# Optimization experiments

Measured on AMD Instinct MI355X. Metric: run time of the kernel, lower is better.

Reference implementation:

```python
import jax, jax.numpy as jnp
import numpy as np

N = 50000       # nodes
E = 1600000     # edges (before self loops)
IN = 128        # in_dim
H = 4           # heads
C = 64          # hidden_channels per head
F = H * C       # 256 concat width
OUT = 10
BN_EPS = 1e-5
NEG_SLOPE = 0.2  # PyG GATConv default


def _gat_conv(x, eidx, W, a_src, a_dst, b):
    # x: [N, F_in]; eidx: [2, E2] with self loops (row0=src, row1=dst)
    xw = (x @ W).reshape(N, H, C)                      # [N, H, C]
    s = jnp.einsum('nhc,hc->nh', xw, a_src)            # [N, H]
    d = jnp.einsum('nhc,hc->nh', xw, a_dst)            # [N, H]
    src, dst = eidx[0], eidx[1]
    alpha = jax.nn.leaky_relu(s[src] + d[dst], NEG_SLOPE)   # [E2, H]
    # scatter-softmax over incoming edges of each dst node (numerically stable)
    m = jax.ops.segment_max(alpha, dst, num_segments=N)
    m = jax.lax.stop_gradient(jnp.where(jnp.isfinite(m), m, 0.0))
    ex = jnp.exp(alpha - m[dst])                       # [E2, H]
    denom = jax.ops.segment_sum(ex, dst, num_segments=N)
    w = ex / (denom[dst] + 1e-16)                      # [E2, H]
    # weighted scatter-add aggregation
    out = jax.ops.segment_sum(w[:, :, None] * xw[src], dst, num_segments=N)  # [N,H,C]
    return out.reshape(N, F) + b


def _batchnorm(h, gamma, beta):
    # training-mode batch stats over the node axis
    mu = jnp.mean(h, axis=0)
    var = jnp.var(h, axis=0)
    return (h - mu) * jax.lax.rsqrt(var + BN_EPS) * gamma + beta


def setup_inputs() -> dict:
    key = jax.random.key(0)
    ks = jax.random.split(key, 12)
    sc = 0.05
    x = jax.random.normal(ks[0], (N, IN), jnp.float32)
    edge_index = jax.random.randint(ks[1], (2, E), 0, N, jnp.int64)
    return {
        'x': x,
        'edge_index': edge_index,
        'W1': jax.random.normal(ks[2], (IN, F), jnp.float32) * sc,
        'a_src1': jax.random.normal(ks[3], (H, C), jnp.float32) * sc,
        'a_dst1': jax.random.normal(ks[4], (H, C), jnp.float32) * sc,
        'b1': jnp.zeros((F,), jnp.float32),
        'W2': jax.random.normal(ks[5], (F, F), jnp.float32) * sc,
        'a_src2': jax.random.normal(ks[6], (H, C), jnp.float32) * sc,
        'a_dst2': jax.random.normal(ks[7], (H, C), jnp.float32) * sc,
        'b2': jnp.zeros((F,), jnp.float32),
        'g1': jnp.ones((F,), jnp.float32),
        'be1': jnp.zeros((F,), jnp.float32),
        'g2': jnp.ones((F,), jnp.float32),
        'be2': jnp.zeros((F,), jnp.float32),
        'Wc': jax.random.normal(ks[8], (F, OUT), jnp.float32) * sc,
        'bc': jnp.zeros((OUT,), jnp.float32),
    }


def reference(x, edge_index, W1, a_src1, a_dst1, b1, W2, a_src2, a_dst2, b2,
              g1, be1, g2, be2, Wc, bc):
    # add self loops (PyG GATConv default add_self_loops=True)
    loops = jnp.arange(N, dtype=edge_index.dtype)
    eidx = jnp.concatenate([edge_index, jnp.stack([loops, loops])], axis=1)
    h = jax.nn.relu(_gat_conv(x, eidx, W1, a_src1, a_dst1, b1))
    h = _batchnorm(h, g1, be1)          # dropout(0.2) treated as identity (eval)
    h = jax.nn.relu(_gat_conv(h, eidx, W2, a_src2, a_dst2, b2))
    h = _batchnorm(h, g2, be2)
    out = h @ Wc + bc                   # [N, OUT]
    return out[None]                    # [1, N, OUT]; squeeze(-1) is a no-op for OUT>1
```

## Files before the change

### kernel.cpp

```cpp
#include <hip/hip_runtime.h>

#define N_NODES 50000
#define E_EDGES 1600000
#define E2 (E_EDGES + N_NODES)
#define HEADS 4
#define F 256
#define OUTC 10
#define BN_EPS 1e-5f
#define NEG_SLOPE 0.2f
#define SB 1024
#define NB ((N_NODES + SB - 1) / SB)
#define NSLICE 64

static_assert(N_NODES % 4 == 0, "grid_nw exact");

typedef __attribute__((ext_vector_type(8))) short short8;
typedef __attribute__((ext_vector_type(4))) float f32x4;

__device__ __forceinline__ unsigned short f2bf(float f) {
    unsigned int u = __float_as_uint(f);
    unsigned int r = (u + 0x7fffu + ((u >> 16) & 1u)) >> 16;
    return (unsigned short)r;
}
__device__ __forceinline__ float bf2f(unsigned short b) {
    return __uint_as_float(((unsigned int)b) << 16);
}

__global__ __launch_bounds__(256) void convert_x(
    const float* __restrict__ X, unsigned short* __restrict__ Xb)
{
    int i = blockIdx.x * blockDim.x + threadIdx.x;
    const int total = N_NODES * 128 / 4;
    if (i >= total) return;
    float4 v = reinterpret_cast<const float4*>(X)[i];
    ushort4 o = { f2bf(v.x), f2bf(v.y), f2bf(v.z), f2bf(v.w) };
    reinterpret_cast<ushort4*>(Xb)[i] = o;
}

__global__ __launch_bounds__(256) void convert_w1T(
    const float* __restrict__ W1, unsigned short* __restrict__ WT)
{
    const int k = blockIdx.x;
    const int n = threadIdx.x;
    WT[n * 128 + k] = f2bf(W1[k * 256 + n]);
}

__global__ __launch_bounds__(256) void count_deg(
    const int* __restrict__ eidx, int* __restrict__ deg)
{
    int e = blockIdx.x * blockDim.x + threadIdx.x;
    if (e >= E2) return;
    int dst = (e < E_EDGES) ? eidx[E_EDGES + e] : e - E_EDGES;
    atomicAdd(&deg[dst], 1);
}

__global__ __launch_bounds__(SB) void scan_blocks(
    const int* __restrict__ deg, int* __restrict__ rowptr, int* __restrict__ bsum)
{
    __shared__ int sm[SB];
    const int t = threadIdx.x;
    const int idx = blockIdx.x * SB + t;
    int v = (idx < N_NODES) ? deg[idx] : 0;
    sm[t] = v;
    __syncthreads();
    for (int off = 1; off < SB; off <<= 1) {
        int u = (t >= off) ? sm[t - off] : 0;
        __syncthreads();
        sm[t] += u;
        __syncthreads();
    }
    if (idx < N_NODES) rowptr[idx] = sm[t] - v;
    if (t == SB - 1) bsum[blockIdx.x] = sm[t];
}

__global__ __launch_bounds__(64) void scan_bsums(
    const int* __restrict__ bsum, int* __restrict__ boff, int* __restrict__ rowptr)
{
    if (threadIdx.x == 0) {
        int run = 0;
        for (int b = 0; b < NB; b++) { boff[b] = run; run += bsum[b]; }
        rowptr[N_NODES] = run;
    }
}

__global__ __launch_bounds__(SB) void scan_add(
    int* __restrict__ rowptr, const int* __restrict__ boff)
{
    const int idx = blockIdx.x * SB + threadIdx.x;
    if (idx < N_NODES) rowptr[idx] += boff[blockIdx.x];
}

__global__ __launch_bounds__(256) void scatter_edges(
    const int* __restrict__ eidx, const int* __restrict__ rowptr,
    int* __restrict__ cursor, int* __restrict__ esrc)
{
    int e = blockIdx.x * blockDim.x + threadIdx.x;
    if (e >= E2) return;
    int src, dst;
    if (e < E_EDGES) { src = eidx[e]; dst = eidx[E_EDGES + e]; }
    else             { src = dst = e - E_EDGES; }
    int pos = atomicAdd(&cursor[dst], 1);
    esrc[rowptr[dst] + pos] = src;
}

template<int K, bool BROW>
__global__ __launch_bounds__(256) void gemm_sd(
    const unsigned short* __restrict__ A, const unsigned short* __restrict__ BT,
    const float* __restrict__ brow, const float* __restrict__ a_src,
    const float* __restrict__ a_dst, unsigned short* __restrict__ C,
    float* __restrict__ S, float* __restrict__ D)
{
    const int t = threadIdx.x;
    const int wave = t >> 6, lane = t & 63;
    const int lo = lane & 15, hi = lane >> 4;
    const int row0 = blockIdx.x * 64;
    const int nbase = wave * 64;

    int arow[4];
#pragma unroll
    for (int m = 0; m < 4; m++)
        arow[m] = min(row0 + m * 16 + lo, N_NODES - 1);

    f32x4 acc[4][4];
#pragma unroll
    for (int m = 0; m < 4; m++)
#pragma unroll
        for (int n = 0; n < 4; n++)
            acc[m][n] = (f32x4){0.f, 0.f, 0.f, 0.f};

    for (int k0 = 0; k0 < K; k0 += 32) {
        const int kk = k0 + hi * 8;
        short8 af[4], bfr[4];
#pragma unroll
        for (int m = 0; m < 4; m++)
            af[m] = *reinterpret_cast<const short8*>(A + (size_t)arow[m] * K + kk);
#pragma unroll
        for (int n = 0; n < 4; n++)
            bfr[n] = *reinterpret_cast<const short8*>(BT + (size_t)(nbase + n * 16 + lo) * K + kk);
#pragma unroll
        for (int m = 0; m < 4; m++)
#pragma unroll
            for (int n = 0; n < 4; n++)
                acc[m][n] = __builtin_amdgcn_mfma_f32_16x16x32_bf16(
                    af[m], bfr[n], acc[m][n], 0, 0, 0);
    }

    float bb[4], asv[4], adv[4];
#pragma unroll
    for (int n = 0; n < 4; n++) {
        int col = nbase + n * 16 + lo;
        bb[n]  = BROW ? brow[col] : 0.f;
        asv[n] = a_src[col];
        adv[n] = a_dst[col];
    }

#pragma unroll
    for (int m = 0; m < 4; m++) {
#pragma unroll
        for (int i = 0; i < 4; i++) {
            const int row = row0 + m * 16 + hi * 4 + i;
            const bool ok = row < N_NODES;
            float ps = 0.f, pd = 0.f;
#pragma unroll
            for (int n = 0; n < 4; n++) {
                float v = acc[m][n][i] + bb[n];
                ps += v * asv[n];
                pd += v * adv[n];
                if (ok) C[(size_t)row * F + nbase + n * 16 + lo] = f2bf(v);
            }
#pragma unroll
            for (int off = 1; off < 16; off <<= 1) {
                ps += __shfl_xor(ps, off, 64);
                pd += __shfl_xor(pd, off, 64);
            }
            if (lo == 0 && ok) {
                S[row * HEADS + wave] = ps;
                D[row * HEADS + wave] = pd;
            }
        }
    }
}

__global__ __launch_bounds__(256) void gat_aggregate(
    const int* __restrict__ rowptr, const int* __restrict__ esrc,
    const float* __restrict__ S, const float* __restrict__ D,
    const unsigned short* __restrict__ XWb, const float* __restrict__ bias,
    unsigned short* __restrict__ Hb, float* __restrict__ stp)
{
    __shared__ int   sbuf[4][64];
    __shared__ float wbuf[4][64][4];
    __shared__ float red_s[4][F];
    __shared__ float red_q[4][F];
    const int wv   = threadIdx.x >> 6;
    const int lane = threadIdx.x & 63;
    const int dst  = blockIdx.x * 4 + wv;
    const int beg = rowptr[dst], end = rowptr[dst + 1];
    const int h = lane >> 4;
    const float4 d4 = *reinterpret_cast<const float4*>(D + dst * HEADS);

    float ax = 0.f, ay = 0.f, az = 0.f, aw = 0.f, den = 0.f;

    for (int i = beg; i < end; i += 64) {
        const int nb = min(64, end - i);
        const bool valid = (i + lane < end);
        const int mysrc = valid ? esrc[i + lane] : 0;
        float4 w4 = {0.f, 0.f, 0.f, 0.f};
        if (valid) {
            const float4 s4 = *reinterpret_cast<const float4*>(S + mysrc * HEADS);
            float z;
            z = s4.x + d4.x; w4.x = __expf(z > 0.f ? z : NEG_SLOPE * z);
            z = s4.y + d4.y; w4.y = __expf(z > 0.f ? z : NEG_SLOPE * z);
            z = s4.z + d4.z; w4.z = __expf(z > 0.f ? z : NEG_SLOPE * z);
            z = s4.w + d4.w; w4.w = __expf(z > 0.f ? z : NEG_SLOPE * z);
        }
        sbuf[wv][lane] = mysrc;
        *reinterpret_cast<float4*>(&wbuf[wv][lane][0]) = w4;

        int j = 0;
        for (; j + 7 < nb; j += 8) {
            int s0 = sbuf[wv][j + 0], s1 = sbuf[wv][j + 1];
            int s2 = sbuf[wv][j + 2], s3 = sbuf[wv][j + 3];
            int s4i = sbuf[wv][j + 4], s5 = sbuf[wv][j + 5];
            int s6 = sbuf[wv][j + 6], s7 = sbuf[wv][j + 7];
            float w0 = wbuf[wv][j + 0][h], w1 = wbuf[wv][j + 1][h];
            float w2 = wbuf[wv][j + 2][h], w3 = wbuf[wv][j + 3][h];
            float w4f = wbuf[wv][j + 4][h], w5 = wbuf[wv][j + 5][h];
            float w6 = wbuf[wv][j + 6][h], w7 = wbuf[wv][j + 7][h];
            ushort4 x0 = *reinterpret_cast<const ushort4*>(XWb + (size_t)s0 * F + lane * 4);
            ushort4 x1 = *reinterpret_cast<const ushort4*>(XWb + (size_t)s1 * F + lane * 4);
            ushort4 x2 = *reinterpret_cast<const ushort4*>(XWb + (size_t)s2 * F + lane * 4);
            ushort4 x3 = *reinterpret_cast<const ushort4*>(XWb + (size_t)s3 * F + lane * 4);
            ushort4 x4 = *reinterpret_cast<const ushort4*>(XWb + (size_t)s4i * F + lane * 4);
            ushort4 x5 = *reinterpret_cast<const ushort4*>(XWb + (size_t)s5 * F + lane * 4);
            ushort4 x6 = *reinterpret_cast<const ushort4*>(XWb + (size_t)s6 * F + lane * 4);
            ushort4 x7 = *reinterpret_cast<const ushort4*>(XWb + (size_t)s7 * F + lane * 4);
            ax += w0 * bf2f(x0.x) + w1 * bf2f(x1.x) + w2 * bf2f(x2.x) + w3 * bf2f(x3.x)
                + w4f * bf2f(x4.x) + w5 * bf2f(x5.x) + w6 * bf2f(x6.x) + w7 * bf2f(x7.x);
            ay += w0 * bf2f(x0.y) + w1 * bf2f(x1.y) + w2 * bf2f(x2.y) + w3 * bf2f(x3.y)
                + w4f * bf2f(x4.y) + w5 * bf2f(x5.y) + w6 * bf2f(x6.y) + w7 * bf2f(x7.y);
            az += w0 * bf2f(x0.z) + w1 * bf2f(x1.z) + w2 * bf2f(x2.z) + w3 * bf2f(x3.z)
                + w4f * bf2f(x4.z) + w5 * bf2f(x5.z) + w6 * bf2f(x6.z) + w7 * bf2f(x7.z);
            aw += w0 * bf2f(x0.w) + w1 * bf2f(x1.w) + w2 * bf2f(x2.w) + w3 * bf2f(x3.w)
                + w4f * bf2f(x4.w) + w5 * bf2f(x5.w) + w6 * bf2f(x6.w) + w7 * bf2f(x7.w);
            den += ((w0 + w1) + (w2 + w3)) + ((w4f + w5) + (w6 + w7));
        }
        for (; j < nb; j++) {
            int   src = sbuf[wv][j];
            float w = wbuf[wv][j][h];
            ushort4 xv = *reinterpret_cast<const ushort4*>(XWb + (size_t)src * F + lane * 4);
            ax += w * bf2f(xv.x); ay += w * bf2f(xv.y);
            az += w * bf2f(xv.z); aw += w * bf2f(xv.w);
            den += w;
        }
    }

    const float inv = 1.f / (den + 1e-16f);
    float4 bv = *reinterpret_cast<const float4*>(bias + lane * 4);
    float v0 = ax * inv + bv.x, v1 = ay * inv + bv.y;
    float v2 = az * inv + bv.z, v3 = aw * inv + bv.w;
    v0 = v0 > 0.f ? v0 : 0.f; v1 = v1 > 0.f ? v1 : 0.f;
    v2 = v2 > 0.f ? v2 : 0.f; v3 = v3 > 0.f ? v3 : 0.f;
    ushort4 o = { f2bf(v0), f2bf(v1), f2bf(v2), f2bf(v3) };
    *reinterpret_cast<ushort4*>(Hb + (size_t)dst * F + lane * 4) = o;

    f32x4 rs = {v0, v1, v2, v3};
    f32x4 rq = {v0 * v0, v1 * v1, v2 * v2, v3 * v3};
    *reinterpret_cast<f32x4*>(&red_s[wv][lane * 4]) = rs;
    *reinterpret_cast<f32x4*>(&red_q[wv][lane * 4]) = rq;
    __syncthreads();
    const int ch = threadIdx.x;
    float s = (red_s[0][ch] + red_s[1][ch]) + (red_s[2][ch] + red_s[3][ch]);
    float q = (red_q[0][ch] + red_q[1][ch]) + (red_q[2][ch] + red_q[3][ch]);
    float* slice = stp + (size_t)(blockIdx.x & (NSLICE - 1)) * (2 * F);
    atomicAdd(&slice[ch], s);
    atomicAdd(&slice[F + ch], q);
}

__global__ __launch_bounds__(256) void prep_brow(
    const float* __restrict__ stp, const float* __restrict__ g,
    const float* __restrict__ be, const float* __restrict__ W2,
    float* __restrict__ scb, float* __restrict__ shb, float* __restrict__ brow)
{
    __shared__ float sh_l[F];
    const int t = threadIdx.x;
    float s = 0.f, q = 0.f;
    for (int b = 0; b < NSLICE; b++) {
        s += stp[(size_t)b * 2 * F + t];
        q += stp[(size_t)b * 2 * F + F + t];
    }
    const float inv_n = 1.f / (float)N_NODES;
    float mu = s * inv_n;
    float var = q * inv_n - mu * mu;
    float sc = rsqrtf(var + BN_EPS) * g[t];
    float sh = be[t] - mu * sc;
    scb[t] = sc;
    shb[t] = sh;
    sh_l[t] = sh;
    __syncthreads();
    float acc = 0.f;
    for (int k = 0; k < F; k++)
        acc += sh_l[k] * W2[(size_t)k * F + t];
    brow[t] = acc;
}

__global__ __launch_bounds__(256) void fold_w2(
    const float* __restrict__ W2, const float* __restrict__ scb,
    unsigned short* __restrict__ WT2b)
{
    const int t = threadIdx.x;
    const int k0 = blockIdx.x * 8;
#pragma unroll
    for (int kk = 0; kk < 8; kk++)
        WT2b[(size_t)t * F + k0 + kk] = f2bf(W2[(size_t)(k0 + kk) * F + t] * scb[k0 + kk]);
}

__global__ __launch_bounds__(256) void fold_wc(
    const float* __restrict__ stp, const float* __restrict__ g,
    const float* __restrict__ be, const float* __restrict__ Wc,
    const float* __restrict__ bc, float* __restrict__ Wcp, float* __restrict__ bcp)
{
    __shared__ float sc_l[F], sh_l[F];
    const int t = threadIdx.x;
    float s = 0.f, q = 0.f;
    for (int b = 0; b < NSLICE; b++) {
        s += stp[(size_t)b * 2 * F + t];
        q += stp[(size_t)b * 2 * F + F + t];
    }
    const float inv_n = 1.f / (float)N_NODES;
    float mu = s * inv_n;
    float var = q * inv_n - mu * mu;
    float sc = rsqrtf(var + BN_EPS) * g[t];
    sc_l[t] = sc;
    sh_l[t] = be[t] - mu * sc;
    __syncthreads();
#pragma unroll
    for (int o = 0; o < OUTC; o++)
        Wcp[t * OUTC + o] = Wc[t * OUTC + o] * sc_l[t];
    if (t < OUTC) {
        float acc = bc[t];
        for (int kk = 0; kk < F; kk++)
            acc += sh_l[kk] * Wc[kk * OUTC + t];
        bcp[t] = acc;
    }
}

__global__ __launch_bounds__(256) void classifier(
    const unsigned short* __restrict__ Hb, const float* __restrict__ Wcp,
    const float* __restrict__ bcp, float* __restrict__ out)
{
    __shared__ float wls[F][OUTC + 1];
    const int t = threadIdx.x;
    for (int i = t; i < F * OUTC; i += 256)
        wls[i / OUTC][i % OUTC] = Wcp[i];
    __syncthreads();

    const int wave = t >> 6, lane = t & 63;
    const int n = blockIdx.x * 4 + wave;
    if (n >= N_NODES) return;

    float v[4];
#pragma unroll
    for (int j = 0; j < 4; j++)
        v[j] = bf2f(Hb[(size_t)n * F + j * 64 + lane]);

    float acc[OUTC];
#pragma unroll
    for (int o = 0; o < OUTC; o++) acc[o] = 0.f;
#pragma unroll
    for (int j = 0; j < 4; j++)
#pragma unroll
        for (int o = 0; o < OUTC; o++)
            acc[o] += v[j] * wls[j * 64 + lane][o];

#pragma unroll
    for (int off = 32; off > 0; off >>= 1)
#pragma unroll
        for (int o = 0; o < OUTC; o++)
            acc[o] += __shfl_xor(acc[o], off, 64);

    if (lane == 0) {
#pragma unroll
        for (int o = 0; o < OUTC; o++)
            out[(size_t)n * OUTC + o] = acc[o] + bcp[o];
    }
}

extern "C" void kernel_launch(void* const* d_in, const int* in_sizes, int n_in,
                              void* d_out, int out_size, void* d_ws, size_t ws_size,
                              hipStream_t stream)
{
    const float* x   = (const float*)d_in[0];
    const int*   ei  = (const int*)d_in[1];
    const float* W1  = (const float*)d_in[2];
    const float* as1 = (const float*)d_in[3];
    const float* ad1 = (const float*)d_in[4];
    const float* b1  = (const float*)d_in[5];
    const float* W2  = (const float*)d_in[6];
    const float* as2 = (const float*)d_in[7];
    const float* ad2 = (const float*)d_in[8];
    const float* b2  = (const float*)d_in[9];
    const float* g1  = (const float*)d_in[10];
    const float* be1 = (const float*)d_in[11];
    const float* g2  = (const float*)d_in[12];
    const float* be2 = (const float*)d_in[13];
    const float* Wc  = (const float*)d_in[14];
    const float* bc  = (const float*)d_in[15];
    float* out = (float*)d_out;

    char* w = (char*)d_ws;
    unsigned short* Xb   = (unsigned short*)w;   w += (size_t)N_NODES * 128 * 2;
    unsigned short* XWb  = (unsigned short*)w;   w += (size_t)N_NODES * F * 2;
    unsigned short* Hb   = (unsigned short*)w;   w += (size_t)N_NODES * F * 2;
    unsigned short* WT1b = (unsigned short*)w;   w += 256 * 128 * 2;
    unsigned short* WT2b = (unsigned short*)w;   w += 256 * 256 * 2;
    float* Wcp   = (float*)w;                    w += F * OUTC * 4;
    float* bcp   = (float*)w;                    w += 64;
    float* brow2 = (float*)w;                    w += F * 4;
    float* scb   = (float*)w;                    w += F * 4;
    float* shb   = (float*)w;                    w += F * 4;
    float* Sv    = (float*)w;                    w += (size_t)N_NODES * HEADS * 4;
    float* Dv    = (float*)w;                    w += (size_t)N_NODES * HEADS * 4;
    float* stp1  = (float*)w;                    w += (size_t)NSLICE * 2 * F * 4;
    float* stp2  = (float*)w;                    w += (size_t)NSLICE * 2 * F * 4;
    int* deg     = (int*)w;                      w += (size_t)N_NODES * 4;
    int* cursor  = (int*)w;                      w += (size_t)N_NODES * 4;
    int* rowp    = (int*)w;                      w += (size_t)(N_NODES + 1) * 4;
    int* bsum    = (int*)w;                      w += NB * 4;
    int* boff    = (int*)w;                      w += NB * 4;
    int* esrc    = (int*)w;

    const int grid_e    = (E2 + 255) / 256;
    const int grid_nw   = N_NODES / 4;
    const int grid_gemm = (N_NODES + 63) / 64;

    hipMemsetAsync(deg, 0, (size_t)N_NODES * 2 * 4, stream);
    hipMemsetAsync(stp1, 0, (size_t)2 * NSLICE * 2 * F * 4, stream);
    convert_x<<<(N_NODES * 128 / 4 + 255) / 256, 256, 0, stream>>>(x, Xb);
    convert_w1T<<<128, 256, 0, stream>>>(W1, WT1b);
    count_deg<<<grid_e, 256, 0, stream>>>(ei, deg);
    scan_blocks<<<NB, SB, 0, stream>>>(deg, rowp, bsum);
    scan_bsums<<<1, 64, 0, stream>>>(bsum, boff, rowp);
    scan_add<<<NB, SB, 0, stream>>>(rowp, boff);
    scatter_edges<<<grid_e, 256, 0, stream>>>(ei, rowp, cursor, esrc);

    gemm_sd<128, false><<<grid_gemm, 256, 0, stream>>>(
        Xb, WT1b, nullptr, as1, ad1, XWb, Sv, Dv);
    gat_aggregate<<<grid_nw, 256, 0, stream>>>(rowp, esrc, Sv, Dv, XWb, b1, Hb, stp1);
    prep_brow<<<1, 256, 0, stream>>>(stp1, g1, be1, W2, scb, shb, brow2);
    fold_w2<<<32, 256, 0, stream>>>(W2, scb, WT2b);

    gemm_sd<256, true><<<grid_gemm, 256, 0, stream>>>(
        Hb, WT2b, brow2, as2, ad2, XWb, Sv, Dv);
    gat_aggregate<<<grid_nw, 256, 0, stream>>>(rowp, esrc, Sv, Dv, XWb, b2, Hb, stp2);
    fold_wc<<<1, 256, 0, stream>>>(stp2, g2, be2, Wc, bc, Wcp, bcp);

    classifier<<<grid_nw, 256, 0, stream>>>(Hb, Wcp, bcp, out);
}
```

Measured before the change: 554.6 us.

## Merge prep kernels, single-block degree scan, fuse BN fold with bias partials

Merges the x conversion, W1 transpose and degree counting into one launch and replaces the three-kernel multi-block scan with a single 1024-thread chunked scan. The BN statistics reduction and bias row computation move into the 32-block W2 fold kernel, which writes 32 partial bias rows that the second GEMM sums in its epilogue. Workspace is reordered so all zeroed buffers sit together and one memset covers them. The aim is fewer launches and less serial single-block work. In exchange, every fold block recomputes the statistics and each GEMM thread does 32 extra loads for the bias.

After: 642.7 us. +15.9%, slower.

```diff
diff --git a/kernel.cpp b/kernel.cpp
--- a/kernel.cpp
+++ b/kernel.cpp
@@ -8,9 +8,13 @@
 #define OUTC 10
 #define BN_EPS 1e-5f
 #define NEG_SLOPE 0.2f
-#define SB 1024
-#define NB ((N_NODES + SB - 1) / SB)
 #define NSLICE 64
+#define SCAN_T 1024
+#define SCAN_CHUNK ((N_NODES + SCAN_T - 1) / SCAN_T)
+
+#define CXB (N_NODES * 128 / 4 / 256)
+#define CWB 128
+#define CDB ((E2 + 255) / 256)
 
 static_assert(N_NODES % 4 == 0, "grid_nw exact");
 
@@ -26,68 +30,55 @@
     return __uint_as_float(((unsigned int)b) << 16);
 }
 
-__global__ __launch_bounds__(256) void convert_x(
-    const float* __restrict__ X, unsigned short* __restrict__ Xb)
-{
-    int i = blockIdx.x * blockDim.x + threadIdx.x;
-    const int total = N_NODES * 128 / 4;
-    if (i >= total) return;
-    float4 v = reinterpret_cast<const float4*>(X)[i];
-    ushort4 o = { f2bf(v.x), f2bf(v.y), f2bf(v.z), f2bf(v.w) };
-    reinterpret_cast<ushort4*>(Xb)[i] = o;
-}
-
-__global__ __launch_bounds__(256) void convert_w1T(
-    const float* __restrict__ W1, unsigned short* __restrict__ WT)
-{
-    const int k = blockIdx.x;
-    const int n = threadIdx.x;
-    WT[n * 128 + k] = f2bf(W1[k * 256 + n]);
-}
-
-__global__ __launch_bounds__(256) void count_deg(
+__global__ __launch_bounds__(256) void mega_prep(
+    const float* __restrict__ X, unsigned short* __restrict__ Xb,
+    const float* __restrict__ W1, unsigned short* __restrict__ WT,
     const int* __restrict__ eidx, int* __restrict__ deg)
 {
-    int e = blockIdx.x * blockDim.x + threadIdx.x;
-    if (e >= E2) return;
-    int dst = (e < E_EDGES) ? eidx[E_EDGES + e] : e - E_EDGES;
-    atomicAdd(&deg[dst], 1);
-}
-
-__global__ __launch_bounds__(SB) void scan_blocks(
-    const int* __restrict__ deg, int* __restrict__ rowptr, int* __restrict__ bsum)
-{
-    __shared__ int sm[SB];
-    const int t = threadIdx.x;
-    const int idx = blockIdx.x * SB + t;
-    int v = (idx < N_NODES) ? deg[idx] : 0;
-    sm[t] = v;
+    const int b = blockIdx.x;
+    const int t = threadIdx.x;
+    if (b < CXB) {
+        const int i = b * 256 + t;
+        float4 v = reinterpret_cast<const float4*>(X)[i];
+        ushort4 o = { f2bf(v.x), f2bf(v.y), f2bf(v.z), f2bf(v.w) };
+        reinterpret_cast<ushort4*>(Xb)[i] = o;
+    } else if (b < CXB + CWB) {
+        const int k = b - CXB;
+        WT[t * 128 + k] = f2bf(W1[k * 256 + t]);
+    } else {
+        const int e = (b - CXB - CWB) * 256 + t;
+        if (e < E2) {
+            int dst = (e < E_EDGES) ? eidx[E_EDGES + e] : e - E_EDGES;
+            atomicAdd(&deg[dst], 1);
+        }
+    }
+}
+
+__global__ __launch_bounds__(SCAN_T) void scan_deg(
+    const int* __restrict__ deg, int* __restrict__ rowptr)
+{
+    __shared__ int part[SCAN_T];
+    const int t = threadIdx.x;
+    const int base = t * SCAN_CHUNK;
+    int s = 0;
+    for (int i = 0; i < SCAN_CHUNK; i++) {
+        int idx = base + i;
+        if (idx < N_NODES) s += deg[idx];
+    }
+    part[t] = s;
     __syncthreads();
-    for (int off = 1; off < SB; off <<= 1) {
-        int u = (t >= off) ? sm[t - off] : 0;
+    for (int off = 1; off < SCAN_T; off <<= 1) {
+        int v = (t >= off) ? part[t - off] : 0;
         __syncthreads();
-        sm[t] += u;
+        part[t] += v;
         __syncthreads();
     }
-    if (idx < N_NODES) rowptr[idx] = sm[t] - v;
-    if (t == SB - 1) bsum[blockIdx.x] = sm[t];
-}
-
-__global__ __launch_bounds__(64) void scan_bsums(
-    const int* __restrict__ bsum, int* __restrict__ boff, int* __restrict__ rowptr)
-{
-    if (threadIdx.x == 0) {
-        int run = 0;
-        for (int b = 0; b < NB; b++) { boff[b] = run; run += bsum[b]; }
-        rowptr[N_NODES] = run;
-    }
-}
-
-__global__ __launch_bounds__(SB) void scan_add(
-    int* __restrict__ rowptr, const int* __restrict__ boff)
-{
-    const int idx = blockIdx.x * SB + threadIdx.x;
-    if (idx < N_NODES) rowptr[idx] += boff[blockIdx.x];
+    int run = (t == 0) ? 0 : part[t - 1];
+    for (int i = 0; i < SCAN_CHUNK; i++) {
+        int idx = base + i;
+        if (idx < N_NODES) { rowptr[idx] = run; run += deg[idx]; }
+    }
+    if (t == 0) rowptr[N_NODES] = part[SCAN_T - 1];
 }
 
 __global__ __launch_bounds__(256) void scatter_edges(
@@ -106,7 +97,7 @@
 template<int K, bool BROW>
 __global__ __launch_bounds__(256) void gemm_sd(
     const unsigned short* __restrict__ A, const unsigned short* __restrict__ BT,
-    const float* __restrict__ brow, const float* __restrict__ a_src,
+    const float* __restrict__ browp, const float* __restrict__ a_src,
     const float* __restrict__ a_dst, unsigned short* __restrict__ C,
     float* __restrict__ S, float* __restrict__ D)
 {
@@ -149,7 +140,11 @@
 #pragma unroll
     for (int n = 0; n < 4; n++) {
         int col = nbase + n * 16 + lo;
-        bb[n]  = BROW ? brow[col] : 0.f;
+        float bbv = 0.f;
+        if (BROW)
+            for (int b = 0; b < 32; b++)
+                bbv += browp[b * F + col];
+        bb[n]  = bbv;
         asv[n] = a_src[col];
         adv[n] = a_dst[col];
     }
@@ -276,12 +271,12 @@
     atomicAdd(&slice[F + ch], q);
 }
 
-__global__ __launch_bounds__(256) void prep_brow(
+__global__ __launch_bounds__(256) void fold_w2b(
     const float* __restrict__ stp, const float* __restrict__ g,
     const float* __restrict__ be, const float* __restrict__ W2,
-    float* __restrict__ scb, float* __restrict__ shb, float* __restrict__ brow)
-{
-    __shared__ float sh_l[F];
+    unsigned short* __restrict__ WT2b, float* __restrict__ browp)
+{
+    __shared__ float sc_l[F], sh_l[F];
     const int t = threadIdx.x;
     float s = 0.f, q = 0.f;
     for (int b = 0; b < NSLICE; b++) {
@@ -292,26 +287,18 @@
     float mu = s * inv_n;
     float var = q * inv_n - mu * mu;
     float sc = rsqrtf(var + BN_EPS) * g[t];
-    float sh = be[t] - mu * sc;
-    scb[t] = sc;
-    shb[t] = sh;
-    sh_l[t] = sh;
+    sc_l[t] = sc;
+    sh_l[t] = be[t] - mu * sc;
     __syncthreads();
-    float acc = 0.f;
-    for (int k = 0; k < F; k++)
-        acc += sh_l[k] * W2[(size_t)k * F + t];
-    brow[t] = acc;
-}
-
-__global__ __launch_bounds__(256) void fold_w2(
-    const float* __restrict__ W2, const float* __restrict__ scb,
-    unsigned short* __restrict__ WT2b)
-{
-    const int t = threadIdx.x;
     const int k0 = blockIdx.x * 8;
-#pragma unroll
-    for (int kk = 0; kk < 8; kk++)
-        WT2b[(size_t)t * F + k0 + kk] = f2bf(W2[(size_t)(k0 + kk) * F + t] * scb[k0 + kk]);
+    float bacc = 0.f;
+#pragma unroll
+    for (int kk = 0; kk < 8; kk++) {
+        float w = W2[(size_t)(k0 + kk) * F + t];
+        WT2b[(size_t)t * F + k0 + kk] = f2bf(w * sc_l[k0 + kk]);
+        bacc += sh_l[k0 + kk] * w;
+    }
+    browp[blockIdx.x * F + t] = bacc;
 }
 
 __global__ __launch_bounds__(256) void fold_wc(
@@ -408,6 +395,12 @@
     float* out = (float*)d_out;
 
     char* w = (char*)d_ws;
+    int*   deg   = (int*)w;                      w += (size_t)N_NODES * 4;
+    int*   cursor= (int*)w;                      w += (size_t)N_NODES * 4;
+    float* stp1  = (float*)w;                    w += (size_t)NSLICE * 2 * F * 4;
+    float* stp2  = (float*)w;                    w += (size_t)NSLICE * 2 * F * 4;
+    const size_t zero_bytes = (size_t)N_NODES * 8 + (size_t)NSLICE * 2 * F * 8;
+
     unsigned short* Xb   = (unsigned short*)w;   w += (size_t)N_NODES * 128 * 2;
     unsigned short* XWb  = (unsigned short*)w;   w += (size_t)N_NODES * F * 2;
     unsigned short* Hb   = (unsigned short*)w;   w += (size_t)N_NODES * F * 2;
@@ -415,42 +408,29 @@
     unsigned short* WT2b = (unsigned short*)w;   w += 256 * 256 * 2;
     float* Wcp   = (float*)w;                    w += F * OUTC * 4;
     float* bcp   = (float*)w;                    w += 64;
-    float* brow2 = (float*)w;                    w += F * 4;
-    float* scb   = (float*)w;                    w += F * 4;
-    float* shb   = (float*)w;                    w += F * 4;
+    float* browp = (float*)w;                    w += 32 * F * 4;
     float* Sv    = (float*)w;                    w += (size_t)N_NODES * HEADS * 4;
     float* Dv    = (float*)w;                    w += (size_t)N_NODES * HEADS * 4;
-    float* stp1  = (float*)w;                    w += (size_t)NSLICE * 2 * F * 4;
-    float* stp2  = (float*)w;                    w += (size_t)NSLICE * 2 * F * 4;
-    int* deg     = (int*)w;                      w += (size_t)N_NODES * 4;
-    int* cursor  = (int*)w;                      w += (size_t)N_NODES * 4;
     int* rowp    = (int*)w;                      w += (size_t)(N_NODES + 1) * 4;
-    int* bsum    = (int*)w;                      w += NB * 4;
-    int* boff    = (int*)w;                      w += NB * 4;
     int* esrc    = (int*)w;
 
     const int grid_e    = (E2 + 255) / 256;
     const int grid_nw   = N_NODES / 4;
     const int grid_gemm = (N_NODES + 63) / 64;
-
-    hipMemsetAsync(deg, 0, (size_t)N_NODES * 2 * 4, stream);
-    hipMemsetAsync(stp1, 0, (size_t)2 * NSLICE * 2 * F * 4, stream);
-    convert_x<<<(N_NODES * 128 / 4 + 255) / 256, 256, 0, stream>>>(x, Xb);
-    convert_w1T<<<128, 256, 0, stream>>>(W1, WT1b);
-    count_deg<<<grid_e, 256, 0, stream>>>(ei, deg);
-    scan_blocks<<<NB, SB, 0, stream>>>(deg, rowp, bsum);
-    scan_bsums<<<1, 64, 0, stream>>>(bsum, boff, rowp);
-    scan_add<<<NB, SB, 0, stream>>>(rowp, boff);
+    const int grid_prep = CXB + CWB + CDB;
+
+    hipMemsetAsync(deg, 0, zero_bytes, stream);
+    mega_prep<<<grid_prep, 256, 0, stream>>>(x, Xb, W1, WT1b, ei, deg);
+    scan_deg<<<1, SCAN_T, 0, stream>>>(deg, rowp);
     scatter_edges<<<grid_e, 256, 0, stream>>>(ei, rowp, cursor, esrc);
 
     gemm_sd<128, false><<<grid_gemm, 256, 0, stream>>>(
         Xb, WT1b, nullptr, as1, ad1, XWb, Sv, Dv);
     gat_aggregate<<<grid_nw, 256, 0, stream>>>(rowp, esrc, Sv, Dv, XWb, b1, Hb, stp1);
-    prep_brow<<<1, 256, 0, stream>>>(stp1, g1, be1, W2, scb, shb, brow2);
-    fold_w2<<<32, 256, 0, stream>>>(W2, scb, WT2b);
+    fold_w2b<<<32, 256, 0, stream>>>(stp1, g1, be1, W2, WT2b, browp);
 
     gemm_sd<256, true><<<grid_gemm, 256, 0, stream>>>(
-        Hb, WT2b, brow2, as2, ad2, XWb, Sv, Dv);
+        Hb, WT2b, browp, as2, ad2, XWb, Sv, Dv);
     gat_aggregate<<<grid_nw, 256, 0, stream>>>(rowp, esrc, Sv, Dv, XWb, b2, Hb, stp2);
     fold_wc<<<1, 256, 0, stream>>>(stp2, g2, be2, Wc, bc, Wcp, bcp);
 
```
